# Performance work log

Hardware: AMD Instinct MI355X
Metric: run time of the kernel (lower is better)

The kernel has to match this reference:

```python
import jax, jax.numpy as jnp
import numpy as np


def setup_inputs() -> dict:
    key = jax.random.key(0)
    k1, k2, k3 = jax.random.split(key, 3)
    shape = (16, 128, 128, 64)  # [B, H, W, C]
    return {
        "query": jax.random.normal(k1, shape, dtype=jnp.float32),
        "keys": jax.random.normal(k2, shape, dtype=jnp.float32),
        "values": jax.random.normal(k3, shape, dtype=jnp.float32),
    }


def reference(query, keys, values):
    # Attention over channel dim C, feature dim = H*W.
    # scores[b, q, k] = sum_{h,w} Q[b,h,w,q] * K[b,h,w,k]
    scores = jnp.einsum("bhwq,bhwk->bqk", query, keys)
    attn = jax.nn.softmax(scores, axis=-1)  # softmax over keys k
    # out[b,h,w,q] = sum_k attn[b,q,k] * V[b,h,w,k]
    out = jnp.einsum("bqk,bhwk->bhwq", attn, values)
    return out
```

## Files before the change

kernel.cpp:

```cpp
#include <hip/hip_runtime.h>


#define TILE_ROWS 32

template <int SPLIT>
__global__ __launch_bounds__(256) void scores_kernel(
    const float* __restrict__ Q, const float* __restrict__ K,
    float* __restrict__ partial) {
  constexpr int CH = 16384 / SPLIT;
  constexpr int NT = CH / TILE_ROWS;
  const int bs = blockIdx.x;
  const int b = bs / SPLIT;
  const int s = bs % SPLIT;
  const int tid = threadIdx.x;
  const int w = tid >> 6;
  const int l = tid & 63;
  const int q0 = (l >> 3) * 8;
  const int k0 = (l & 7) * 8;

  __shared__ union {
    float4 buf[4][2][256];
    float red[2][4096];
  } lds;

  float acc[8][8];
#pragma unroll
  for (int i = 0; i < 8; ++i)
#pragma unroll
    for (int j = 0; j < 8; ++j) acc[i][j] = 0.f;

  const float4* Qg = (const float4*)(Q + ((size_t)b * 16384 + (size_t)s * CH) * 64);
  const float4* Kg = (const float4*)(K + ((size_t)b * 16384 + (size_t)s * CH) * 64);

  const int i0 = l >> 4;
  const int c0 = l & 15;
  const int gq0 = (4 * i0 + w) * 16 + c0;
  const int gq1 = gq0 + 256;

  lds.buf[w][0][l]       = Qg[gq0];
  lds.buf[w][0][64 + l]  = Qg[gq1];
  lds.buf[w][0][128 + l] = Kg[gq0];
  lds.buf[w][0][192 + l] = Kg[gq1];

  for (int t = 0; t < NT; ++t) {
    const int cb = t & 1;

    float4 pq0, pq1, pk0, pk1;
    if (t + 1 < NT) {
      pq0 = Qg[(t + 1) * 512 + gq0];
      pq1 = Qg[(t + 1) * 512 + gq1];
      pk0 = Kg[(t + 1) * 512 + gq0];
      pk1 = Kg[(t + 1) * 512 + gq1];
    }

    const float4* qp = lds.buf[w][cb];
    const float4* kp = lds.buf[w][cb] + 128;
#pragma unroll
    for (int i = 0; i < 8; ++i) {
      float4 qa = qp[i * 16 + (q0 >> 2)];
      float4 qb = qp[i * 16 + (q0 >> 2) + 1];
      float4 ka = kp[i * 16 + (k0 >> 2)];
      float4 kb = kp[i * 16 + (k0 >> 2) + 1];
      float qv[8] = {qa.x, qa.y, qa.z, qa.w, qb.x, qb.y, qb.z, qb.w};
      float kv[8] = {ka.x, ka.y, ka.z, ka.w, kb.x, kb.y, kb.z, kb.w};
#pragma unroll
      for (int ii = 0; ii < 8; ++ii)
#pragma unroll
        for (int jj = 0; jj < 8; ++jj)
          acc[ii][jj] += qv[ii] * kv[jj];
    }

    if (t + 1 < NT) {
      const int nb = (t + 1) & 1;
      lds.buf[w][nb][l]       = pq0;
      lds.buf[w][nb][64 + l]  = pq1;
      lds.buf[w][nb][128 + l] = pk0;
      lds.buf[w][nb][192 + l] = pk1;
    }
  }

  __syncthreads();
  if (w >= 2) {
    float4* dst = (float4*)lds.red[w - 2];
#pragma unroll
    for (int i = 0; i < 8; ++i) {
      dst[(q0 + i) * 16 + (k0 >> 2)]     = make_float4(acc[i][0], acc[i][1], acc[i][2], acc[i][3]);
      dst[(q0 + i) * 16 + (k0 >> 2) + 1] = make_float4(acc[i][4], acc[i][5], acc[i][6], acc[i][7]);
    }
  }
  __syncthreads();
  if (w < 2) {
    float4* dst = (float4*)lds.red[w];
#pragma unroll
    for (int i = 0; i < 8; ++i) {
      float4 u = dst[(q0 + i) * 16 + (k0 >> 2)];
      float4 v = dst[(q0 + i) * 16 + (k0 >> 2) + 1];
      dst[(q0 + i) * 16 + (k0 >> 2)]     = make_float4(u.x + acc[i][0], u.y + acc[i][1], u.z + acc[i][2], u.w + acc[i][3]);
      dst[(q0 + i) * 16 + (k0 >> 2) + 1] = make_float4(v.x + acc[i][4], v.y + acc[i][5], v.z + acc[i][6], v.w + acc[i][7]);
    }
  }
  __syncthreads();
  float4* p4 = (float4*)(partial + (size_t)bs * 4096);
  const float4* r0 = (const float4*)lds.red[0];
  const float4* r1 = (const float4*)lds.red[1];
#pragma unroll
  for (int c = 0; c < 4; ++c) {
    float4 x = r0[c * 256 + tid];
    float4 y = r1[c * 256 + tid];
    p4[c * 256 + tid] = make_float4(x.x + y.x, x.y + y.y, x.z + y.z, x.w + y.w);
  }
}

template <int SPLIT>
__global__ __launch_bounds__(256) void softmax_kernel(
    const float* __restrict__ partial, float* __restrict__ attn_t) {
  const int blk = blockIdx.x;
  const int b = blk >> 4;
  const int q0 = (blk & 15) * 4;
  const int tid = threadIdx.x;
  const int w = tid >> 6;
  const int l = tid & 63;
  const int ql = l >> 4;
  const int k4 = l & 15;

  __shared__ float4 red4[4][64];

  const float4* P = (const float4*)partial;
  float4 v = make_float4(0.f, 0.f, 0.f, 0.f);
  for (int s = w; s < SPLIT; s += 4) {
    float4 t = P[((size_t)(b * SPLIT + s) * 64 + q0 + ql) * 16 + k4];
    v.x += t.x; v.y += t.y; v.z += t.z; v.w += t.w;
  }
  red4[w][l] = v;
  __syncthreads();
  if (w != 0) return;

  float4 v1 = red4[1][l], v2 = red4[2][l], v3 = red4[3][l];
  v.x += v1.x + v2.x + v3.x;
  v.y += v1.y + v2.y + v3.y;
  v.z += v1.z + v2.z + v3.z;
  v.w += v1.w + v2.w + v3.w;

  float m = fmaxf(fmaxf(v.x, v.y), fmaxf(v.z, v.w));
#pragma unroll
  for (int off = 8; off > 0; off >>= 1)
    m = fmaxf(m, __shfl_xor(m, off, 64));
  float4 e = make_float4(__expf(v.x - m), __expf(v.y - m), __expf(v.z - m), __expf(v.w - m));
  float sum = e.x + e.y + e.z + e.w;
#pragma unroll
  for (int off = 8; off > 0; off >>= 1)
    sum += __shfl_xor(sum, off, 64);
  const float inv = 1.f / sum;

  float* A = attn_t + (size_t)b * 4096;
  A[(4 * k4 + 0) * 64 + q0 + ql] = e.x * inv;
  A[(4 * k4 + 1) * 64 + q0 + ql] = e.y * inv;
  A[(4 * k4 + 2) * 64 + q0 + ql] = e.z * inv;
  A[(4 * k4 + 3) * 64 + q0 + ql] = e.w * inv;
}

__global__ __launch_bounds__(256) void out_kernel(
    const float* __restrict__ V, const float* __restrict__ attn_t,
    float* __restrict__ out) {
  const int b = blockIdx.x >> 6;
  const int tile = blockIdx.x & 63;
  const int tid = threadIdx.x;
  const int w = tid >> 6;
  const int l = tid & 63;
  const int rg = l >> 3;
  const int qg = l & 7;

  __shared__ float4 Vl[256 * 16];
  __shared__ float4 Al[64 * 16];

  const float4* Vg = (const float4*)(V + ((size_t)b * 16384 + (size_t)tile * 256) * 64);
#pragma unroll
  for (int u = 0; u < 16; ++u) {
    const int n = u * 256 + tid;
    const int r = n >> 4, c = n & 15;
    Vl[(r << 4) | (c ^ (r & 7))] = Vg[n];
  }
  const float4* Ag = (const float4*)(attn_t + (size_t)b * 4096);
#pragma unroll
  for (int u = 0; u < 4; ++u)
    Al[u * 256 + tid] = Ag[u * 256 + tid];
  __syncthreads();

  float acc[8][8];
#pragma unroll
  for (int i = 0; i < 8; ++i)
#pragma unroll
    for (int j = 0; j < 8; ++j) acc[i][j] = 0.f;

#pragma unroll 2
  for (int k4 = 0; k4 < 16; ++k4) {
    float4 alo[4], ahi[4];
#pragma unroll
    for (int j = 0; j < 4; ++j) {
      alo[j] = Al[(4 * k4 + j) * 16 + qg];
      ahi[j] = Al[(4 * k4 + j) * 16 + 8 + qg];
    }
#pragma unroll
    for (int i = 0; i < 8; ++i) {
      const int row = (w << 6) + rg + 8 * i;
      const float4 v = Vl[(row << 4) | (k4 ^ rg)];
      acc[i][0] += v.x * alo[0].x + v.y * alo[1].x + v.z * alo[2].x + v.w * alo[3].x;
      acc[i][1] += v.x * alo[0].y + v.y * alo[1].y + v.z * alo[2].y + v.w * alo[3].y;
      acc[i][2] += v.x * alo[0].z + v.y * alo[1].z + v.z * alo[2].z + v.w * alo[3].z;
      acc[i][3] += v.x * alo[0].w + v.y * alo[1].w + v.z * alo[2].w + v.w * alo[3].w;
      acc[i][4] += v.x * ahi[0].x + v.y * ahi[1].x + v.z * ahi[2].x + v.w * ahi[3].x;
      acc[i][5] += v.x * ahi[0].y + v.y * ahi[1].y + v.z * ahi[2].y + v.w * ahi[3].y;
      acc[i][6] += v.x * ahi[0].z + v.y * ahi[1].z + v.z * ahi[2].z + v.w * ahi[3].z;
      acc[i][7] += v.x * ahi[0].w + v.y * ahi[1].w + v.z * ahi[2].w + v.w * ahi[3].w;
    }
  }

  float4* og = (float4*)(out + ((size_t)b * 16384 + (size_t)tile * 256) * 64);
#pragma unroll
  for (int i = 0; i < 8; ++i) {
    const int row = (w << 6) + rg + 8 * i;
    og[row * 16 + qg]     = make_float4(acc[i][0], acc[i][1], acc[i][2], acc[i][3]);
    og[row * 16 + 8 + qg] = make_float4(acc[i][4], acc[i][5], acc[i][6], acc[i][7]);
  }
}

extern "C" void kernel_launch(void* const* d_in, const int* in_sizes, int n_in,
                              void* d_out, int out_size, void* d_ws, size_t ws_size,
                              hipStream_t stream) {
  const float* Q = (const float*)d_in[0];
  const float* K = (const float*)d_in[1];
  const float* V = (const float*)d_in[2];
  float* out = (float*)d_out;

  const size_t need64 = (size_t)16 * 64 * 4096 * 4 + (size_t)16 * 4096 * 4;

  if (ws_size >= need64) {
    float* partial = (float*)d_ws;
    float* attn_t = partial + (size_t)16 * 64 * 4096;
    scores_kernel<64><<<16 * 64, 256, 0, stream>>>(Q, K, partial);
    softmax_kernel<64><<<16 * 16, 256, 0, stream>>>(partial, attn_t);
    out_kernel<<<16 * 64, 256, 0, stream>>>(V, attn_t, out);
  } else {
    float* partial = (float*)d_ws;
    float* attn_t = partial + (size_t)16 * 32 * 4096;
    scores_kernel<32><<<16 * 32, 256, 0, stream>>>(Q, K, partial);
    softmax_kernel<32><<<16 * 16, 256, 0, stream>>>(partial, attn_t);
    out_kernel<<<16 * 64, 256, 0, stream>>>(V, attn_t, out);
  }
}
```

Baseline: 237.4 us.

## Use split-bf16 MFMA for the QK^T scores kernel

Replaces the scalar FP32 outer-product accumulation in the scores kernel with bf16 MFMA 16x16x32 instructions. Q and K are split into high and low bf16 parts (three products per tile) to keep near-FP32 accuracy, and are staged transposed in swizzled LDS. Each wave now owns a 16-row slice of the 64x64 scores tile, so the cross-wave LDS reduction is removed and partials are written directly. The cost is extra conversion work per staged element and a block-wide barrier every iteration; the dropped low-by-low term reduces accuracy slightly.

New measurement: 238.6 us. No clear change (+0.5%).

```diff
diff --git a/kernel.cpp b/kernel.cpp
--- a/kernel.cpp
+++ b/kernel.cpp
@@ -1,113 +1,121 @@
 #include <hip/hip_runtime.h>
 
 
-#define TILE_ROWS 32
+typedef __attribute__((ext_vector_type(8))) short bf16x8;
+typedef __attribute__((ext_vector_type(4))) float f32x4;
+
+__device__ __forceinline__ unsigned short f2bf(float x) {
+  unsigned u = __builtin_bit_cast(unsigned, x);
+  u += 0x7FFFu + ((u >> 16) & 1u);
+  return (unsigned short)(u >> 16);
+}
+__device__ __forceinline__ float bf2f(unsigned short h) {
+  unsigned u = (unsigned)h << 16;
+  return __builtin_bit_cast(float, u);
+}
 
 template <int SPLIT>
 __global__ __launch_bounds__(256) void scores_kernel(
     const float* __restrict__ Q, const float* __restrict__ K,
     float* __restrict__ partial) {
   constexpr int CH = 16384 / SPLIT;
-  constexpr int NT = CH / TILE_ROWS;
+  constexpr int NTT = CH / 64;
   const int bs = blockIdx.x;
   const int b = bs / SPLIT;
   const int s = bs % SPLIT;
   const int tid = threadIdx.x;
   const int w = tid >> 6;
   const int l = tid & 63;
-  const int q0 = (l >> 3) * 8;
-  const int k0 = (l & 7) * 8;
-
-  __shared__ union {
-    float4 buf[4][2][256];
-    float red[2][4096];
-  } lds;
-
-  float acc[8][8];
-#pragma unroll
-  for (int i = 0; i < 8; ++i)
-#pragma unroll
-    for (int j = 0; j < 8; ++j) acc[i][j] = 0.f;
+
+  __shared__ unsigned short T[2][4][64][64];
 
   const float4* Qg = (const float4*)(Q + ((size_t)b * 16384 + (size_t)s * CH) * 64);
   const float4* Kg = (const float4*)(K + ((size_t)b * 16384 + (size_t)s * CH) * 64);
 
-  const int i0 = l >> 4;
-  const int c0 = l & 15;
-  const int gq0 = (4 * i0 + w) * 16 + c0;
-  const int gq1 = gq0 + 256;
-
-  lds.buf[w][0][l]       = Qg[gq0];
-  lds.buf[w][0][64 + l]  = Qg[gq1];
-  lds.buf[w][0][128 + l] = Kg[gq0];
-  lds.buf[w][0][192 + l] = Kg[gq1];
-
-  for (int t = 0; t < NT; ++t) {
+  const int half = tid >> 7;
+  const int c4 = tid & 15;
+  const int hq0 = (tid >> 4) & 7;
+  const float4* Sg = half ? Kg : Qg;
+  const int arrH = half ? 2 : 0, arrL = half ? 3 : 1;
+
+  auto stage_load = [&](int t, int hq, float4& r0, float4& r1, float4& r2, float4& r3) {
+    const float4* src = Sg + (size_t)(t * 64 + 4 * hq) * 16 + c4;
+    r0 = src[0]; r1 = src[16]; r2 = src[32]; r3 = src[48];
+  };
+  auto stage_write = [&](int buf, int hq, float4 r0, float4 r1, float4 r2, float4 r3) {
+    const float* p0 = (const float*)&r0; const float* p1 = (const float*)&r1;
+    const float* p2 = (const float*)&r2; const float* p3 = (const float*)&r3;
+#pragma unroll
+    for (int j = 0; j < 4; ++j) {
+      const int c = 4 * c4 + j;
+      const float v0 = p0[j], v1 = p1[j], v2 = p2[j], v3 = p3[j];
+      const unsigned short h0 = f2bf(v0), h1 = f2bf(v1), h2 = f2bf(v2), h3 = f2bf(v3);
+      const unsigned short g0 = f2bf(v0 - bf2f(h0)), g1 = f2bf(v1 - bf2f(h1));
+      const unsigned short g2 = f2bf(v2 - bf2f(h2)), g3 = f2bf(v3 - bf2f(h3));
+      const int hqs = hq ^ ((c & 7) << 1);
+      *(uint2*)&T[buf][arrH][c][4 * hqs] =
+          make_uint2((unsigned)h0 | ((unsigned)h1 << 16), (unsigned)h2 | ((unsigned)h3 << 16));
+      *(uint2*)&T[buf][arrL][c][4 * hqs] =
+          make_uint2((unsigned)g0 | ((unsigned)g1 << 16), (unsigned)g2 | ((unsigned)g3 << 16));
+    }
+  };
+  auto frag = [&](int buf, int arr, int row, int step) -> bf16x8 {
+    const int e = (step * 32 + ((l >> 4) << 3)) ^ ((row & 7) << 3);
+    return *(const bf16x8*)&T[buf][arr][row][e];
+  };
+
+  f32x4 acc[4] = {};
+
+  {
+    float4 a0, a1, a2, a3, b0, b1, b2, b3;
+    stage_load(0, hq0, a0, a1, a2, a3);
+    stage_load(0, hq0 + 8, b0, b1, b2, b3);
+    stage_write(0, hq0, a0, a1, a2, a3);
+    stage_write(0, hq0 + 8, b0, b1, b2, b3);
+  }
+
+  const int arow = w * 16 + (l & 15);
+  const int bcol = l & 15;
+
+  for (int t = 0; t < NTT; ++t) {
+    __syncthreads();
     const int cb = t & 1;
 
-    float4 pq0, pq1, pk0, pk1;
-    if (t + 1 < NT) {
-      pq0 = Qg[(t + 1) * 512 + gq0];
-      pq1 = Qg[(t + 1) * 512 + gq1];
-      pk0 = Kg[(t + 1) * 512 + gq0];
-      pk1 = Kg[(t + 1) * 512 + gq1];
-    }
-
-    const float4* qp = lds.buf[w][cb];
-    const float4* kp = lds.buf[w][cb] + 128;
-#pragma unroll
-    for (int i = 0; i < 8; ++i) {
-      float4 qa = qp[i * 16 + (q0 >> 2)];
-      float4 qb = qp[i * 16 + (q0 >> 2) + 1];
-      float4 ka = kp[i * 16 + (k0 >> 2)];
-      float4 kb = kp[i * 16 + (k0 >> 2) + 1];
-      float qv[8] = {qa.x, qa.y, qa.z, qa.w, qb.x, qb.y, qb.z, qb.w};
-      float kv[8] = {ka.x, ka.y, ka.z, ka.w, kb.x, kb.y, kb.z, kb.w};
-#pragma unroll
-      for (int ii = 0; ii < 8; ++ii)
-#pragma unroll
-        for (int jj = 0; jj < 8; ++jj)
-          acc[ii][jj] += qv[ii] * kv[jj];
-    }
-
-    if (t + 1 < NT) {
+    float4 a0, a1, a2, a3, b0, b1, b2, b3;
+    if (t + 1 < NTT) {
+      stage_load(t + 1, hq0, a0, a1, a2, a3);
+      stage_load(t + 1, hq0 + 8, b0, b1, b2, b3);
+    }
+
+#pragma unroll
+    for (int step = 0; step < 2; ++step) {
+      const bf16x8 ah = frag(cb, 0, arow, step);
+      const bf16x8 al = frag(cb, 1, arow, step);
+#pragma unroll
+      for (int kt = 0; kt < 4; ++kt) {
+        const bf16x8 bh = frag(cb, 2, kt * 16 + bcol, step);
+        const bf16x8 bl = frag(cb, 3, kt * 16 + bcol, step);
+        acc[kt] = __builtin_amdgcn_mfma_f32_16x16x32_bf16(ah, bh, acc[kt], 0, 0, 0);
+        acc[kt] = __builtin_amdgcn_mfma_f32_16x16x32_bf16(ah, bl, acc[kt], 0, 0, 0);
+        acc[kt] = __builtin_amdgcn_mfma_f32_16x16x32_bf16(al, bh, acc[kt], 0, 0, 0);
+      }
+    }
+
+    if (t + 1 < NTT) {
       const int nb = (t + 1) & 1;
-      lds.buf[w][nb][l]       = pq0;
-      lds.buf[w][nb][64 + l]  = pq1;
-      lds.buf[w][nb][128 + l] = pk0;
-      lds.buf[w][nb][192 + l] = pk1;
-    }
-  }
-
-  __syncthreads();
-  if (w >= 2) {
-    float4* dst = (float4*)lds.red[w - 2];
-#pragma unroll
-    for (int i = 0; i < 8; ++i) {
-      dst[(q0 + i) * 16 + (k0 >> 2)]     = make_float4(acc[i][0], acc[i][1], acc[i][2], acc[i][3]);
-      dst[(q0 + i) * 16 + (k0 >> 2) + 1] = make_float4(acc[i][4], acc[i][5], acc[i][6], acc[i][7]);
-    }
-  }
-  __syncthreads();
-  if (w < 2) {
-    float4* dst = (float4*)lds.red[w];
-#pragma unroll
-    for (int i = 0; i < 8; ++i) {
-      float4 u = dst[(q0 + i) * 16 + (k0 >> 2)];
-      float4 v = dst[(q0 + i) * 16 + (k0 >> 2) + 1];
-      dst[(q0 + i) * 16 + (k0 >> 2)]     = make_float4(u.x + acc[i][0], u.y + acc[i][1], u.z + acc[i][2], u.w + acc[i][3]);
-      dst[(q0 + i) * 16 + (k0 >> 2) + 1] = make_float4(v.x + acc[i][4], v.y + acc[i][5], v.z + acc[i][6], v.w + acc[i][7]);
-    }
-  }
-  __syncthreads();
-  float4* p4 = (float4*)(partial + (size_t)bs * 4096);
-  const float4* r0 = (const float4*)lds.red[0];
-  const float4* r1 = (const float4*)lds.red[1];
-#pragma unroll
-  for (int c = 0; c < 4; ++c) {
-    float4 x = r0[c * 256 + tid];
-    float4 y = r1[c * 256 + tid];
-    p4[c * 256 + tid] = make_float4(x.x + y.x, x.y + y.y, x.z + y.z, x.w + y.w);
+      stage_write(nb, hq0, a0, a1, a2, a3);
+      stage_write(nb, hq0 + 8, b0, b1, b2, b3);
+    }
+  }
+
+  float* P = partial + (size_t)bs * 4096;
+#pragma unroll
+  for (int kt = 0; kt < 4; ++kt) {
+#pragma unroll
+    for (int r = 0; r < 4; ++r) {
+      const int q = w * 16 + ((l >> 4) << 2) + r;
+      P[q * 64 + kt * 16 + (l & 15)] = acc[kt][r];
+    }
   }
 }
 
```
